# Kernel tuning notes

Hardware: AMD Instinct MI355X
Metric: run time of the kernel (lower is better)

The kernel has to match this reference:

```python
import jax, jax.numpy as jnp
import numpy as np

N_NODES = 50000
N_EDGES = 800000
IN_SIZE = 128
HIDDEN = 128   # out_size * 2
OUT_SIZE = 64


def setup_inputs() -> dict:
    key = jax.random.key(0)
    ks = jax.random.split(key, 6)
    h = jax.random.normal(ks[0], (N_NODES, IN_SIZE), dtype=jnp.float32)
    W1 = jax.random.normal(ks[1], (IN_SIZE, HIDDEN), dtype=jnp.float32) * (1.0 / np.sqrt(IN_SIZE))
    b1 = jnp.zeros((HIDDEN,), dtype=jnp.float32)
    W2 = jax.random.normal(ks[2], (HIDDEN, OUT_SIZE), dtype=jnp.float32) * (1.0 / np.sqrt(HIDDEN))
    b2 = jnp.zeros((OUT_SIZE,), dtype=jnp.float32)
    src = jax.random.randint(ks[3], (N_EDGES,), 0, N_NODES, dtype=jnp.int64)
    dst = jax.random.randint(ks[4], (N_EDGES,), 0, N_NODES, dtype=jnp.int64)
    return {"h": h, "W1": W1, "b1": b1, "W2": W2, "b2": b2, "src": src, "dst": dst}


def _norms(src, dst, n_nodes):
    # DGL GraphConv norm='both': scale by out_degree^{-1/2} (src side)
    # and in_degree^{-1/2} (dst side); zero degrees clamped to 1.
    ones = jnp.ones(src.shape, dtype=jnp.float32)
    out_deg = jnp.maximum(jax.ops.segment_sum(ones, src, num_segments=n_nodes), 1.0)
    in_deg = jnp.maximum(jax.ops.segment_sum(ones, dst, num_segments=n_nodes), 1.0)
    return (out_deg ** -0.5)[:, None], (in_deg ** -0.5)[:, None]


def _graph_conv(x, W, b, src, dst, norm_out, norm_in, n_nodes):
    # h' = D_in^{-1/2} A D_out^{-1/2} x W + b
    x = x * norm_out                                   # [N, F]
    agg = jax.ops.segment_sum(x[src], dst, num_segments=n_nodes)  # SpMM: [N, F]
    return (agg * norm_in) @ W + b


def reference(h, W1, b1, W2, b2, src, dst):
    n_nodes = h.shape[0]
    norm_out, norm_in = _norms(src, dst, n_nodes)
    h = jax.nn.relu(_graph_conv(h, W1, b1, src, dst, norm_out, norm_in, n_nodes))
    h = jax.nn.relu(_graph_conv(h, W2, b2, src, dst, norm_out, norm_in, n_nodes))
    return h
```

## Files before the change

kernel.cpp:

```cpp
#include <hip/hip_runtime.h>

#define N_NODES 50000
#define N_EDGES 800000
#define IN_SIZE 128
#define HIDDEN 128
#define OUT_SIZE 64

#define CHUNKS 128
#define CHUNK_EDGES 6250
#define GEMMA_TILES 1563
#define NBS 196

static __device__ inline unsigned pack_bf16x2(float a, float b) {
    unsigned ua = __float_as_uint(a);
    unsigned ub = __float_as_uint(b);
    unsigned ra = (ua + 0x7fffu + ((ua >> 16) & 1u)) >> 16;
    unsigned rb = (ub + 0x7fffu + ((ub >> 16) & 1u)) & 0xffff0000u;
    return ra | rb;
}

static __device__ inline unsigned pack_f16x2(float a, float b) {
    _Float16 ha = (_Float16)a, hb = (_Float16)b;
    unsigned short ua = __builtin_bit_cast(unsigned short, ha);
    unsigned short ub = __builtin_bit_cast(unsigned short, hb);
    return (unsigned)ua | ((unsigned)ub << 16);
}

static __device__ inline float2 unpack_f16x2(unsigned u) {
    _Float16 lo = __builtin_bit_cast(_Float16, (unsigned short)(u & 0xffffu));
    _Float16 hi = __builtin_bit_cast(_Float16, (unsigned short)(u >> 16));
    return make_float2((float)lo, (float)hi);
}

__global__ __launch_bounds__(1024) void hist_kernel(const int* __restrict__ src,
                                                    const int* __restrict__ dst,
                                                    unsigned char* __restrict__ cntD,
                                                    unsigned char* __restrict__ cntS,
                                                    unsigned char* __restrict__ rp) {
    __shared__ unsigned hD[12500];
    __shared__ unsigned hS[12500];
    const int t = threadIdx.x;
    const int c = blockIdx.x;

    for (int i = t; i < 12500; i += 1024) { hD[i] = 0u; hS[i] = 0u; }
    __syncthreads();

    const int base = c * CHUNK_EDGES;
    for (int i = t; i < CHUNK_EDGES; i += 1024) {
        int e = base + i;
        int d = dst[e];
        int s = src[e];
        unsigned shd = (unsigned)(d & 3) * 8u;
        unsigned old = atomicAdd(&hD[d >> 2], 1u << shd);
        rp[e] = (unsigned char)((old >> shd) & 0xffu);
        atomicAdd(&hS[s >> 2], 1u << ((unsigned)(s & 3) * 8u));
    }
    __syncthreads();

    unsigned* gD = (unsigned*)cntD + (size_t)c * 12500;
    unsigned* gS = (unsigned*)cntS + (size_t)c * 12500;
    for (int i = t; i < 12500; i += 1024) { gD[i] = hD[i]; gS[i] = hS[i]; }
}

__global__ __launch_bounds__(256) void deg_scan_kernel(unsigned char* __restrict__ cntD,
                                                       const unsigned char* __restrict__ cntS,
                                                       int* __restrict__ row_ptr,
                                                       int* __restrict__ bsum,
                                                       float* __restrict__ norm_out,
                                                       float* __restrict__ norm_in) {
    const int t = threadIdx.x, lane = t & 63, w = t >> 6;
    const int n = blockIdx.x * 256 + t;
    unsigned sumD = 0u, sumS = 0u;
    if (n < N_NODES) {
        #pragma unroll 4
        for (int c = 0; c < CHUNKS; ++c) {
            size_t idx = (size_t)c * 50000 + n;
            unsigned v = cntD[idx];
            cntD[idx] = (unsigned char)sumD;
            sumD += v;
            sumS += cntS[idx];
        }
        norm_in[n]  = rsqrtf((float)(sumD ? sumD : 1u));
        norm_out[n] = rsqrtf((float)(sumS ? sumS : 1u));
    }
    __shared__ int wsum[4];
    int v = (n < N_NODES) ? (int)sumD : 0;
    int incl = v;
    #pragma unroll
    for (int d = 1; d < 64; d <<= 1) {
        int u = __shfl_up(incl, d, 64);
        if (lane >= d) incl += u;
    }
    if (lane == 63) wsum[w] = incl;
    __syncthreads();
    int woff = 0, total = 0;
    #pragma unroll
    for (int j = 0; j < 4; ++j) {
        int s = wsum[j];
        if (j < w) woff += s;
        total += s;
    }
    if (n < N_NODES) row_ptr[n] = woff + incl - v;
    if (t == 0) bsum[blockIdx.x] = total;
}

__global__ __launch_bounds__(64) void scan2_kernel(int* __restrict__ bsum,
                                                   int* __restrict__ row_ptr) {
    const int lane = threadIdx.x;
    int carry = 0;
    for (int base = 0; base < NBS; base += 64) {
        int t = base + lane;
        int v = (t < NBS) ? bsum[t] : 0;
        int incl = v;
        #pragma unroll
        for (int d = 1; d < 64; d <<= 1) {
            int u = __shfl_up(incl, d, 64);
            if (lane >= d) incl += u;
        }
        int excl = carry + incl - v;
        if (t < NBS) bsum[t] = excl;
        if (t == NBS - 1) row_ptr[N_NODES] = N_EDGES - excl;
        carry += __shfl(incl, 63, 64);
    }
}

__global__ __launch_bounds__(256) void gemmA_kernel(const float* __restrict__ h,
                                                    const float* __restrict__ W1,
                                                    unsigned short* __restrict__ t1) {
    __shared__ float sA[32][128];
    __shared__ float sW[32][128];

    const int tile = blockIdx.x;
    const int t  = threadIdx.x;
    const int tx = t & 31;
    const int ty = t >> 5;
    const int n0 = tile * 32;

    for (int i = t; i < 1024; i += 256) {
        int n = i >> 5, c = i & 31;
        int gn = n0 + n;
        float4 v = make_float4(0.f, 0.f, 0.f, 0.f);
        if (gn < N_NODES) v = ((const float4*)(h + (size_t)gn * 128))[c];
        ((float4*)sA[n])[c] = v;
    }

    float4 acc[4];
    #pragma unroll
    for (int i = 0; i < 4; ++i) acc[i] = make_float4(0.f, 0.f, 0.f, 0.f);

    for (int kc = 0; kc < 4; ++kc) {
        __syncthreads();
        for (int i = t; i < 1024; i += 256) {
            int k = i >> 5, c = i & 31;
            ((float4*)sW[k])[c] = ((const float4*)(W1 + (size_t)(kc * 32 + k) * 128))[c];
        }
        __syncthreads();
        #pragma unroll 8
        for (int k = 0; k < 32; ++k) {
            float4 w = ((float4*)sW[k])[tx];
            #pragma unroll
            for (int ni = 0; ni < 4; ++ni) {
                float a = sA[ty * 4 + ni][kc * 32 + k];
                acc[ni].x = fmaf(a, w.x, acc[ni].x);
                acc[ni].y = fmaf(a, w.y, acc[ni].y);
                acc[ni].z = fmaf(a, w.z, acc[ni].z);
                acc[ni].w = fmaf(a, w.w, acc[ni].w);
            }
        }
    }

    #pragma unroll
    for (int ni = 0; ni < 4; ++ni) {
        int gn = n0 + ty * 4 + ni;
        if (gn < N_NODES) {
            uint2 p;
            p.x = pack_bf16x2(acc[ni].x, acc[ni].y);
            p.y = pack_bf16x2(acc[ni].z, acc[ni].w);
            ((uint2*)(t1 + (size_t)gn * 128))[tx] = p;
        }
    }
}

__global__ __launch_bounds__(256) void place_kernel(const int* __restrict__ src,
                                                    const int* __restrict__ dst,
                                                    const int* __restrict__ row_ptr,
                                                    const int* __restrict__ bsum,
                                                    const unsigned char* __restrict__ cntD,
                                                    const unsigned char* __restrict__ rp,
                                                    int* __restrict__ eidx) {
    int e = blockIdx.x * 256 + threadIdx.x;
    if (e < N_EDGES) {
        int d = dst[e];
        int c = e / CHUNK_EDGES;
        int pos = row_ptr[d] + bsum[d >> 8] + (int)cntD[(size_t)c * 50000 + d] + (int)rp[e];
        eidx[pos] = src[e];
    }
}

__global__ __launch_bounds__(256) void gemmB_kernel(const float* __restrict__ h1p,
                                                    const float* __restrict__ W2,
                                                    unsigned short* __restrict__ t2h) {
    __shared__ float sA[32][128];
    __shared__ float sW[128][64];
    const int t  = threadIdx.x;
    const int tx = t & 15;
    const int ty = t >> 4;
    const int n0 = blockIdx.x * 32;

    for (int i = t; i < 1024; i += 256) {
        int n = i >> 5, c = i & 31;
        int gn = n0 + n;
        float4 v = make_float4(0.f, 0.f, 0.f, 0.f);
        if (gn < N_NODES) v = ((const float4*)(h1p + (size_t)gn * 128))[c];
        ((float4*)sA[n])[c] = v;
    }
    for (int i = t; i < 2048; i += 256) {
        int k = i >> 4, c = i & 15;
        ((float4*)sW[k])[c] = ((const float4*)(W2 + (size_t)k * 64))[c];
    }
    __syncthreads();

    float4 a0 = make_float4(0.f, 0.f, 0.f, 0.f);
    float4 a1 = make_float4(0.f, 0.f, 0.f, 0.f);
    #pragma unroll 8
    for (int k = 0; k < 128; ++k) {
        float4 w = ((float4*)sW[k])[tx];
        float x0 = sA[ty * 2 + 0][k];
        float x1 = sA[ty * 2 + 1][k];
        a0.x = fmaf(x0, w.x, a0.x); a0.y = fmaf(x0, w.y, a0.y);
        a0.z = fmaf(x0, w.z, a0.z); a0.w = fmaf(x0, w.w, a0.w);
        a1.x = fmaf(x1, w.x, a1.x); a1.y = fmaf(x1, w.y, a1.y);
        a1.z = fmaf(x1, w.z, a1.z); a1.w = fmaf(x1, w.w, a1.w);
    }

    #pragma unroll
    for (int ni = 0; ni < 2; ++ni) {
        int gn = n0 + ty * 2 + ni;
        if (gn < N_NODES) {
            float4 a = ni ? a1 : a0;
            uint2 p;
            p.x = pack_f16x2(a.x, a.y);
            p.y = pack_f16x2(a.z, a.w);
            ((uint2*)(t2h + (size_t)gn * 64))[tx] = p;
        }
    }
}

__global__ __launch_bounds__(256) void pull128_kernel(const unsigned short* __restrict__ xb,
                                                      const int* __restrict__ row_ptr,
                                                      const int* __restrict__ bsum,
                                                      const int* __restrict__ eidx,
                                                      const float* __restrict__ b1,
                                                      const float* __restrict__ norm_in,
                                                      const float* __restrict__ norm_out,
                                                      float* __restrict__ out) {
    int node = blockIdx.x * 4 + (threadIdx.x >> 6);
    node = __builtin_amdgcn_readfirstlane(node);
    const int lane = threadIdx.x & 63;
    const int beg = __builtin_amdgcn_readfirstlane(row_ptr[node] + bsum[node >> 8]);
    const int end = __builtin_amdgcn_readfirstlane(row_ptr[node + 1] + bsum[(node + 1) >> 8]);

    float2 acc0 = make_float2(0.f, 0.f);
    float2 acc1 = make_float2(0.f, 0.f);
    float2 acc2 = make_float2(0.f, 0.f);
    float2 acc3 = make_float2(0.f, 0.f);

    for (int base = beg; base < end; base += 64) {
        const int cnt = min(64, end - base);
        int my_e = 0;
        float my_n = 0.f;
        if (lane < cnt) {
            my_e = eidx[base + lane];
            my_n = norm_out[my_e];
        }
        int k = 0;
        for (; k + 7 < cnt; k += 8) {
            int s0 = __builtin_amdgcn_readlane(my_e, k);
            int s1 = __builtin_amdgcn_readlane(my_e, k + 1);
            int s2 = __builtin_amdgcn_readlane(my_e, k + 2);
            int s3 = __builtin_amdgcn_readlane(my_e, k + 3);
            int s4 = __builtin_amdgcn_readlane(my_e, k + 4);
            int s5 = __builtin_amdgcn_readlane(my_e, k + 5);
            int s6 = __builtin_amdgcn_readlane(my_e, k + 6);
            int s7 = __builtin_amdgcn_readlane(my_e, k + 7);
            float n0 = __int_as_float(__builtin_amdgcn_readlane(__float_as_int(my_n), k));
            float n1 = __int_as_float(__builtin_amdgcn_readlane(__float_as_int(my_n), k + 1));
            float n2 = __int_as_float(__builtin_amdgcn_readlane(__float_as_int(my_n), k + 2));
            float n3 = __int_as_float(__builtin_amdgcn_readlane(__float_as_int(my_n), k + 3));
            float n4 = __int_as_float(__builtin_amdgcn_readlane(__float_as_int(my_n), k + 4));
            float n5 = __int_as_float(__builtin_amdgcn_readlane(__float_as_int(my_n), k + 5));
            float n6 = __int_as_float(__builtin_amdgcn_readlane(__float_as_int(my_n), k + 6));
            float n7 = __int_as_float(__builtin_amdgcn_readlane(__float_as_int(my_n), k + 7));
            unsigned u0 = ((const unsigned*)(xb + (size_t)s0 * 128))[lane];
            unsigned u1 = ((const unsigned*)(xb + (size_t)s1 * 128))[lane];
            unsigned u2 = ((const unsigned*)(xb + (size_t)s2 * 128))[lane];
            unsigned u3 = ((const unsigned*)(xb + (size_t)s3 * 128))[lane];
            unsigned u4 = ((const unsigned*)(xb + (size_t)s4 * 128))[lane];
            unsigned u5 = ((const unsigned*)(xb + (size_t)s5 * 128))[lane];
            unsigned u6 = ((const unsigned*)(xb + (size_t)s6 * 128))[lane];
            unsigned u7 = ((const unsigned*)(xb + (size_t)s7 * 128))[lane];
            acc0.x = fmaf(__uint_as_float(u0 << 16), n0, acc0.x);
            acc0.y = fmaf(__uint_as_float(u0 & 0xffff0000u), n0, acc0.y);
            acc1.x = fmaf(__uint_as_float(u1 << 16), n1, acc1.x);
            acc1.y = fmaf(__uint_as_float(u1 & 0xffff0000u), n1, acc1.y);
            acc2.x = fmaf(__uint_as_float(u2 << 16), n2, acc2.x);
            acc2.y = fmaf(__uint_as_float(u2 & 0xffff0000u), n2, acc2.y);
            acc3.x = fmaf(__uint_as_float(u3 << 16), n3, acc3.x);
            acc3.y = fmaf(__uint_as_float(u3 & 0xffff0000u), n3, acc3.y);
            acc0.x = fmaf(__uint_as_float(u4 << 16), n4, acc0.x);
            acc0.y = fmaf(__uint_as_float(u4 & 0xffff0000u), n4, acc0.y);
            acc1.x = fmaf(__uint_as_float(u5 << 16), n5, acc1.x);
            acc1.y = fmaf(__uint_as_float(u5 & 0xffff0000u), n5, acc1.y);
            acc2.x = fmaf(__uint_as_float(u6 << 16), n6, acc2.x);
            acc2.y = fmaf(__uint_as_float(u6 & 0xffff0000u), n6, acc2.y);
            acc3.x = fmaf(__uint_as_float(u7 << 16), n7, acc3.x);
            acc3.y = fmaf(__uint_as_float(u7 & 0xffff0000u), n7, acc3.y);
        }
        for (; k + 3 < cnt; k += 4) {
            int s0 = __builtin_amdgcn_readlane(my_e, k);
            int s1 = __builtin_amdgcn_readlane(my_e, k + 1);
            int s2 = __builtin_amdgcn_readlane(my_e, k + 2);
            int s3 = __builtin_amdgcn_readlane(my_e, k + 3);
            float n0 = __int_as_float(__builtin_amdgcn_readlane(__float_as_int(my_n), k));
            float n1 = __int_as_float(__builtin_amdgcn_readlane(__float_as_int(my_n), k + 1));
            float n2 = __int_as_float(__builtin_amdgcn_readlane(__float_as_int(my_n), k + 2));
            float n3 = __int_as_float(__builtin_amdgcn_readlane(__float_as_int(my_n), k + 3));
            unsigned u0 = ((const unsigned*)(xb + (size_t)s0 * 128))[lane];
            unsigned u1 = ((const unsigned*)(xb + (size_t)s1 * 128))[lane];
            unsigned u2 = ((const unsigned*)(xb + (size_t)s2 * 128))[lane];
            unsigned u3 = ((const unsigned*)(xb + (size_t)s3 * 128))[lane];
            acc0.x = fmaf(__uint_as_float(u0 << 16), n0, acc0.x);
            acc0.y = fmaf(__uint_as_float(u0 & 0xffff0000u), n0, acc0.y);
            acc1.x = fmaf(__uint_as_float(u1 << 16), n1, acc1.x);
            acc1.y = fmaf(__uint_as_float(u1 & 0xffff0000u), n1, acc1.y);
            acc2.x = fmaf(__uint_as_float(u2 << 16), n2, acc2.x);
            acc2.y = fmaf(__uint_as_float(u2 & 0xffff0000u), n2, acc2.y);
            acc3.x = fmaf(__uint_as_float(u3 << 16), n3, acc3.x);
            acc3.y = fmaf(__uint_as_float(u3 & 0xffff0000u), n3, acc3.y);
        }
        for (; k < cnt; ++k) {
            int s0 = __builtin_amdgcn_readlane(my_e, k);
            float n0 = __int_as_float(__builtin_amdgcn_readlane(__float_as_int(my_n), k));
            unsigned u0 = ((const unsigned*)(xb + (size_t)s0 * 128))[lane];
            acc0.x = fmaf(__uint_as_float(u0 << 16), n0, acc0.x);
            acc0.y = fmaf(__uint_as_float(u0 & 0xffff0000u), n0, acc0.y);
        }
    }

    float ni = norm_in[node];
    float no = norm_out[node];
    float2 bb = ((const float2*)b1)[lane];
    float sx = (acc0.x + acc1.x) + (acc2.x + acc3.x);
    float sy = (acc0.y + acc1.y) + (acc2.y + acc3.y);
    float2 r;
    r.x = fmaxf(fmaf(sx, ni, bb.x), 0.f) * no;
    r.y = fmaxf(fmaf(sy, ni, bb.y), 0.f) * no;
    ((float2*)(out + (size_t)node * 128))[lane] = r;
}

__global__ __launch_bounds__(256) void pull64_kernel(const unsigned* __restrict__ x,
                                                     const int* __restrict__ row_ptr,
                                                     const int* __restrict__ bsum,
                                                     const int* __restrict__ eidx,
                                                     const float* __restrict__ b2,
                                                     const float* __restrict__ norm_in,
                                                     float* __restrict__ out) {
    int node = blockIdx.x * 4 + (threadIdx.x >> 6);
    node = __builtin_amdgcn_readfirstlane(node);
    const int lane = threadIdx.x & 63;
    const int half = lane >> 5;
    const int fl = lane & 31;
    const int beg = __builtin_amdgcn_readfirstlane(row_ptr[node] + bsum[node >> 8]);
    const int end = __builtin_amdgcn_readfirstlane(row_ptr[node + 1] + bsum[(node + 1) >> 8]);

    float2 a0 = make_float2(0.f, 0.f);
    float2 a1 = make_float2(0.f, 0.f);
    float2 a2 = make_float2(0.f, 0.f);
    float2 a3 = make_float2(0.f, 0.f);

    for (int base = beg; base < end; base += 64) {
        const int cnt = min(64, end - base);
        int my_e = (lane < cnt) ? eidx[base + lane] : 0;
        int k = 0;
        for (; k + 7 < cnt; k += 8) {
            int sa0 = __builtin_amdgcn_readlane(my_e, k);
            int sb0 = __builtin_amdgcn_readlane(my_e, k + 1);
            int sa1 = __builtin_amdgcn_readlane(my_e, k + 2);
            int sb1 = __builtin_amdgcn_readlane(my_e, k + 3);
            int sa2 = __builtin_amdgcn_readlane(my_e, k + 4);
            int sb2 = __builtin_amdgcn_readlane(my_e, k + 5);
            int sa3 = __builtin_amdgcn_readlane(my_e, k + 6);
            int sb3 = __builtin_amdgcn_readlane(my_e, k + 7);
            int e0 = half ? sb0 : sa0;
            int e1 = half ? sb1 : sa1;
            int e2 = half ? sb2 : sa2;
            int e3 = half ? sb3 : sa3;
            unsigned u0 = x[(size_t)e0 * 32 + fl];
            unsigned u1 = x[(size_t)e1 * 32 + fl];
            unsigned u2 = x[(size_t)e2 * 32 + fl];
            unsigned u3 = x[(size_t)e3 * 32 + fl];
            float2 v0 = unpack_f16x2(u0);
            float2 v1 = unpack_f16x2(u1);
            float2 v2 = unpack_f16x2(u2);
            float2 v3 = unpack_f16x2(u3);
            a0.x += v0.x; a0.y += v0.y;
            a1.x += v1.x; a1.y += v1.y;
            a2.x += v2.x; a2.y += v2.y;
            a3.x += v3.x; a3.y += v3.y;
        }
        for (; k + 1 < cnt; k += 2) {
            int sa = __builtin_amdgcn_readlane(my_e, k);
            int sb = __builtin_amdgcn_readlane(my_e, k + 1);
            int e0 = half ? sb : sa;
            unsigned u = x[(size_t)e0 * 32 + fl];
            float2 v = unpack_f16x2(u);
            a0.x += v.x; a0.y += v.y;
        }
        if (k < cnt) {
            int sa = __builtin_amdgcn_readlane(my_e, k);
            if (half == 0) {
                unsigned u = x[(size_t)sa * 32 + fl];
                float2 v = unpack_f16x2(u);
                a0.x += v.x; a0.y += v.y;
            }
        }
    }

    float ax = (a0.x + a1.x) + (a2.x + a3.x);
    float ay = (a0.y + a1.y) + (a2.y + a3.y);
    ax += __shfl_xor(ax, 32, 64);
    ay += __shfl_xor(ay, 32, 64);
    if (half == 0) {
        float ni = norm_in[node];
        float2 bb = ((const float2*)b2)[fl];
        float2 r;
        r.x = fmaxf(fmaf(ax, ni, bb.x), 0.f);
        r.y = fmaxf(fmaf(ay, ni, bb.y), 0.f);
        ((float2*)(out + (size_t)node * 64))[fl] = r;
    }
}

extern "C" void kernel_launch(void* const* d_in, const int* in_sizes, int n_in,
                              void* d_out, int out_size, void* d_ws, size_t ws_size,
                              hipStream_t stream) {
    const float* h  = (const float*)d_in[0];
    const float* W1 = (const float*)d_in[1];
    const float* b1 = (const float*)d_in[2];
    const float* W2 = (const float*)d_in[3];
    const float* b2 = (const float*)d_in[4];
    const int* src  = (const int*)d_in[5];
    const int* dst  = (const int*)d_in[6];
    float* out = (float*)d_out;

    char* ws = (char*)d_ws;
    size_t off = 0;
    auto alloc = [&](size_t bytes) {
        void* p = ws + off;
        off = (off + bytes + 255) & ~(size_t)255;
        return p;
    };
    float* norm_out   = (float*)alloc(N_NODES * sizeof(float));
    float* norm_in    = (float*)alloc(N_NODES * sizeof(float));
    int* row_ptr      = (int*)alloc((N_NODES + 1) * sizeof(int));
    int* bsum         = (int*)alloc(NBS * sizeof(int));
    int* eidx         = (int*)alloc((size_t)N_EDGES * sizeof(int));
    unsigned short* t1 = (unsigned short*)alloc((size_t)N_NODES * 128 * sizeof(short));
    float* h1p        = (float*)alloc((size_t)N_NODES * 128 * sizeof(float));

    unsigned char* cntD = (unsigned char*)h1p;
    unsigned char* cntS = cntD + (size_t)CHUNKS * 50000;
    unsigned char* rp   = cntS + (size_t)CHUNKS * 50000;
    unsigned short* t2h = t1;

    hist_kernel<<<CHUNKS, 1024, 0, stream>>>(src, dst, cntD, cntS, rp);

    gemmA_kernel<<<GEMMA_TILES, 256, 0, stream>>>(h, W1, t1);

    deg_scan_kernel<<<NBS, 256, 0, stream>>>(cntD, cntS, row_ptr, bsum, norm_out, norm_in);

    scan2_kernel<<<1, 64, 0, stream>>>(bsum, row_ptr);

    place_kernel<<<(N_EDGES + 255) / 256, 256, 0, stream>>>(src, dst, row_ptr, bsum, cntD, rp, eidx);

    pull128_kernel<<<N_NODES / 4, 256, 0, stream>>>(t1, row_ptr, bsum, eidx, b1,
                                                    norm_in, norm_out, h1p);

    gemmB_kernel<<<(N_NODES + 31) / 32, 256, 0, stream>>>(h1p, W2, t2h);
    pull64_kernel<<<N_NODES / 4, 256, 0, stream>>>((const unsigned*)t2h, row_ptr, bsum, eidx,
                                                   b2, norm_in, out);
}
```

Baseline: 227.1 us.

## Fuse histogram and first GEMM into one launch; half-wave edge split in pull128

Merges the edge histogram kernel and the first dense transform into a single launch: low block indices build per-chunk histograms, the rest compute four 32-row GEMM tiles each using partitioned 128KB shared memory. This lets the histogram work overlap with the GEMM and removes a launch. The 128-wide gather kernel now has each half-wave process a different edge with 8-byte loads, then combines the halves via a cross-lane shuffle. This gives fewer load instructions per edge, at the cost of a reduction and larger per-block shared memory.

```diff
diff --git a/kernel.cpp b/kernel.cpp
--- a/kernel.cpp
+++ b/kernel.cpp
@@ -9,6 +9,8 @@
 #define CHUNKS 128
 #define CHUNK_EDGES 6250
 #define GEMMA_TILES 1563
+#define GEMMA_SUPER 391
+#define FUSED_GRID (CHUNKS + GEMMA_SUPER)
 #define NBS 196
 
 static __device__ inline unsigned pack_bf16x2(float a, float b) {
@@ -32,34 +34,98 @@
     return make_float2((float)lo, (float)hi);
 }
 
-__global__ __launch_bounds__(1024) void hist_kernel(const int* __restrict__ src,
-                                                    const int* __restrict__ dst,
-                                                    unsigned char* __restrict__ cntD,
-                                                    unsigned char* __restrict__ cntS,
-                                                    unsigned char* __restrict__ rp) {
-    __shared__ unsigned hD[12500];
-    __shared__ unsigned hS[12500];
-    const int t = threadIdx.x;
-    const int c = blockIdx.x;
-
-    for (int i = t; i < 12500; i += 1024) { hD[i] = 0u; hS[i] = 0u; }
-    __syncthreads();
-
-    const int base = c * CHUNK_EDGES;
-    for (int i = t; i < CHUNK_EDGES; i += 1024) {
-        int e = base + i;
-        int d = dst[e];
-        int s = src[e];
-        unsigned shd = (unsigned)(d & 3) * 8u;
-        unsigned old = atomicAdd(&hD[d >> 2], 1u << shd);
-        rp[e] = (unsigned char)((old >> shd) & 0xffu);
-        atomicAdd(&hS[s >> 2], 1u << ((unsigned)(s & 3) * 8u));
-    }
-    __syncthreads();
-
-    unsigned* gD = (unsigned*)cntD + (size_t)c * 12500;
-    unsigned* gS = (unsigned*)cntS + (size_t)c * 12500;
-    for (int i = t; i < 12500; i += 1024) { gD[i] = hD[i]; gS[i] = hS[i]; }
+static __device__ inline float bf_lo(unsigned w) { return __uint_as_float(w << 16); }
+static __device__ inline float bf_hi(unsigned w) { return __uint_as_float(w & 0xffff0000u); }
+
+__global__ __launch_bounds__(1024) void fused_hist_gemmA(const int* __restrict__ src,
+                                                         const int* __restrict__ dst,
+                                                         unsigned char* __restrict__ cntD,
+                                                         unsigned char* __restrict__ cntS,
+                                                         unsigned char* __restrict__ rp,
+                                                         const float* __restrict__ h,
+                                                         const float* __restrict__ W1,
+                                                         unsigned short* __restrict__ t1) {
+    __shared__ __align__(16) unsigned char smem[131072];
+    const int b = blockIdx.x;
+
+    if (b < CHUNKS) {
+        unsigned* hD = (unsigned*)smem;
+        unsigned* hS = hD + 12500;
+        const int t = threadIdx.x;
+        for (int i = t; i < 12500; i += 1024) { hD[i] = 0u; hS[i] = 0u; }
+        __syncthreads();
+        const int base = b * CHUNK_EDGES;
+        for (int i = t; i < CHUNK_EDGES; i += 1024) {
+            int e = base + i;
+            int d = dst[e];
+            int s = src[e];
+            unsigned shd = (unsigned)(d & 3) * 8u;
+            unsigned old = atomicAdd(&hD[d >> 2], 1u << shd);
+            rp[e] = (unsigned char)((old >> shd) & 0xffu);
+            atomicAdd(&hS[s >> 2], 1u << ((unsigned)(s & 3) * 8u));
+        }
+        __syncthreads();
+        unsigned* gD = (unsigned*)cntD + (size_t)b * 12500;
+        unsigned* gS = (unsigned*)cntS + (size_t)b * 12500;
+        for (int i = t; i < 12500; i += 1024) { gD[i] = hD[i]; gS[i] = hS[i]; }
+        return;
+    }
+
+    const int sub = threadIdx.x >> 8;
+    const int t   = threadIdx.x & 255;
+    int tile = (b - CHUNKS) * 4 + sub;
+    if (tile >= GEMMA_TILES) tile = GEMMA_TILES - 1;
+
+    float* sA = (float*)(smem + (size_t)sub * 32768);
+    float* sW = sA + 32 * 128;
+
+    const int tx = t & 31;
+    const int ty = t >> 5;
+    const int n0 = tile * 32;
+
+    for (int i = t; i < 1024; i += 256) {
+        int n = i >> 5, c = i & 31;
+        int gn = n0 + n;
+        float4 v = make_float4(0.f, 0.f, 0.f, 0.f);
+        if (gn < N_NODES) v = ((const float4*)(h + (size_t)gn * 128))[c];
+        ((float4*)(sA + n * 128))[c] = v;
+    }
+
+    float4 acc[4];
+    #pragma unroll
+    for (int i = 0; i < 4; ++i) acc[i] = make_float4(0.f, 0.f, 0.f, 0.f);
+
+    for (int kc = 0; kc < 4; ++kc) {
+        __syncthreads();
+        for (int i = t; i < 1024; i += 256) {
+            int k = i >> 5, c = i & 31;
+            ((float4*)(sW + k * 128))[c] = ((const float4*)(W1 + (size_t)(kc * 32 + k) * 128))[c];
+        }
+        __syncthreads();
+        #pragma unroll 8
+        for (int k = 0; k < 32; ++k) {
+            float4 w = ((float4*)(sW + k * 128))[tx];
+            #pragma unroll
+            for (int ni = 0; ni < 4; ++ni) {
+                float a = sA[(ty * 4 + ni) * 128 + kc * 32 + k];
+                acc[ni].x = fmaf(a, w.x, acc[ni].x);
+                acc[ni].y = fmaf(a, w.y, acc[ni].y);
+                acc[ni].z = fmaf(a, w.z, acc[ni].z);
+                acc[ni].w = fmaf(a, w.w, acc[ni].w);
+            }
+        }
+    }
+
+    #pragma unroll
+    for (int ni = 0; ni < 4; ++ni) {
+        int gn = n0 + ty * 4 + ni;
+        if (gn < N_NODES) {
+            uint2 p;
+            p.x = pack_bf16x2(acc[ni].x, acc[ni].y);
+            p.y = pack_bf16x2(acc[ni].z, acc[ni].w);
+            ((uint2*)(t1 + (size_t)gn * 128))[tx] = p;
+        }
+    }
 }
 
 __global__ __launch_bounds__(256) void deg_scan_kernel(unsigned char* __restrict__ cntD,
@@ -124,63 +190,6 @@
     }
 }
 
-__global__ __launch_bounds__(256) void gemmA_kernel(const float* __restrict__ h,
-                                                    const float* __restrict__ W1,
-                                                    unsigned short* __restrict__ t1) {
-    __shared__ float sA[32][128];
-    __shared__ float sW[32][128];
-
-    const int tile = blockIdx.x;
-    const int t  = threadIdx.x;
-    const int tx = t & 31;
-    const int ty = t >> 5;
-    const int n0 = tile * 32;
-
-    for (int i = t; i < 1024; i += 256) {
-        int n = i >> 5, c = i & 31;
-        int gn = n0 + n;
-        float4 v = make_float4(0.f, 0.f, 0.f, 0.f);
-        if (gn < N_NODES) v = ((const float4*)(h + (size_t)gn * 128))[c];
-        ((float4*)sA[n])[c] = v;
-    }
-
-    float4 acc[4];
-    #pragma unroll
-    for (int i = 0; i < 4; ++i) acc[i] = make_float4(0.f, 0.f, 0.f, 0.f);
-
-    for (int kc = 0; kc < 4; ++kc) {
-        __syncthreads();
-        for (int i = t; i < 1024; i += 256) {
-            int k = i >> 5, c = i & 31;
-            ((float4*)sW[k])[c] = ((const float4*)(W1 + (size_t)(kc * 32 + k) * 128))[c];
-        }
-        __syncthreads();
-        #pragma unroll 8
-        for (int k = 0; k < 32; ++k) {
-            float4 w = ((float4*)sW[k])[tx];
-            #pragma unroll
-            for (int ni = 0; ni < 4; ++ni) {
-                float a = sA[ty * 4 + ni][kc * 32 + k];
-                acc[ni].x = fmaf(a, w.x, acc[ni].x);
-                acc[ni].y = fmaf(a, w.y, acc[ni].y);
-                acc[ni].z = fmaf(a, w.z, acc[ni].z);
-                acc[ni].w = fmaf(a, w.w, acc[ni].w);
-            }
-        }
-    }
-
-    #pragma unroll
-    for (int ni = 0; ni < 4; ++ni) {
-        int gn = n0 + ty * 4 + ni;
-        if (gn < N_NODES) {
-            uint2 p;
-            p.x = pack_bf16x2(acc[ni].x, acc[ni].y);
-            p.y = pack_bf16x2(acc[ni].z, acc[ni].w);
-            ((uint2*)(t1 + (size_t)gn * 128))[tx] = p;
-        }
-    }
-}
-
 __global__ __launch_bounds__(256) void place_kernel(const int* __restrict__ src,
                                                     const int* __restrict__ dst,
                                                     const int* __restrict__ row_ptr,
@@ -257,13 +266,15 @@
     int node = blockIdx.x * 4 + (threadIdx.x >> 6);
     node = __builtin_amdgcn_readfirstlane(node);
     const int lane = threadIdx.x & 63;
+    const int half = lane >> 5;
+    const int fl = lane & 31;
     const int beg = __builtin_amdgcn_readfirstlane(row_ptr[node] + bsum[node >> 8]);
     const int end = __builtin_amdgcn_readfirstlane(row_ptr[node + 1] + bsum[(node + 1) >> 8]);
 
-    float2 acc0 = make_float2(0.f, 0.f);
-    float2 acc1 = make_float2(0.f, 0.f);
-    float2 acc2 = make_float2(0.f, 0.f);
-    float2 acc3 = make_float2(0.f, 0.f);
+    float4 acc0 = make_float4(0.f, 0.f, 0.f, 0.f);
+    float4 acc1 = make_float4(0.f, 0.f, 0.f, 0.f);
+    float4 acc2 = make_float4(0.f, 0.f, 0.f, 0.f);
+    float4 acc3 = make_float4(0.f, 0.f, 0.f, 0.f);
 
     for (int base = beg; base < end; base += 64) {
         const int cnt = min(64, end - base);
@@ -275,87 +286,92 @@
         }
         int k = 0;
         for (; k + 7 < cnt; k += 8) {
-            int s0 = __builtin_amdgcn_readlane(my_e, k);
-            int s1 = __builtin_amdgcn_readlane(my_e, k + 1);
-            int s2 = __builtin_amdgcn_readlane(my_e, k + 2);
-            int s3 = __builtin_amdgcn_readlane(my_e, k + 3);
-            int s4 = __builtin_amdgcn_readlane(my_e, k + 4);
-            int s5 = __builtin_amdgcn_readlane(my_e, k + 5);
-            int s6 = __builtin_amdgcn_readlane(my_e, k + 6);
-            int s7 = __builtin_amdgcn_readlane(my_e, k + 7);
-            float n0 = __int_as_float(__builtin_amdgcn_readlane(__float_as_int(my_n), k));
-            float n1 = __int_as_float(__builtin_amdgcn_readlane(__float_as_int(my_n), k + 1));
-            float n2 = __int_as_float(__builtin_amdgcn_readlane(__float_as_int(my_n), k + 2));
-            float n3 = __int_as_float(__builtin_amdgcn_readlane(__float_as_int(my_n), k + 3));
-            float n4 = __int_as_float(__builtin_amdgcn_readlane(__float_as_int(my_n), k + 4));
-            float n5 = __int_as_float(__builtin_amdgcn_readlane(__float_as_int(my_n), k + 5));
-            float n6 = __int_as_float(__builtin_amdgcn_readlane(__float_as_int(my_n), k + 6));
-            float n7 = __int_as_float(__builtin_amdgcn_readlane(__float_as_int(my_n), k + 7));
-            unsigned u0 = ((const unsigned*)(xb + (size_t)s0 * 128))[lane];
-            unsigned u1 = ((const unsigned*)(xb + (size_t)s1 * 128))[lane];
-            unsigned u2 = ((const unsigned*)(xb + (size_t)s2 * 128))[lane];
-            unsigned u3 = ((const unsigned*)(xb + (size_t)s3 * 128))[lane];
-            unsigned u4 = ((const unsigned*)(xb + (size_t)s4 * 128))[lane];
-            unsigned u5 = ((const unsigned*)(xb + (size_t)s5 * 128))[lane];
-            unsigned u6 = ((const unsigned*)(xb + (size_t)s6 * 128))[lane];
-            unsigned u7 = ((const unsigned*)(xb + (size_t)s7 * 128))[lane];
-            acc0.x = fmaf(__uint_as_float(u0 << 16), n0, acc0.x);
-            acc0.y = fmaf(__uint_as_float(u0 & 0xffff0000u), n0, acc0.y);
-            acc1.x = fmaf(__uint_as_float(u1 << 16), n1, acc1.x);
-            acc1.y = fmaf(__uint_as_float(u1 & 0xffff0000u), n1, acc1.y);
-            acc2.x = fmaf(__uint_as_float(u2 << 16), n2, acc2.x);
-            acc2.y = fmaf(__uint_as_float(u2 & 0xffff0000u), n2, acc2.y);
-            acc3.x = fmaf(__uint_as_float(u3 << 16), n3, acc3.x);
-            acc3.y = fmaf(__uint_as_float(u3 & 0xffff0000u), n3, acc3.y);
-            acc0.x = fmaf(__uint_as_float(u4 << 16), n4, acc0.x);
-            acc0.y = fmaf(__uint_as_float(u4 & 0xffff0000u), n4, acc0.y);
-            acc1.x = fmaf(__uint_as_float(u5 << 16), n5, acc1.x);
-            acc1.y = fmaf(__uint_as_float(u5 & 0xffff0000u), n5, acc1.y);
-            acc2.x = fmaf(__uint_as_float(u6 << 16), n6, acc2.x);
-            acc2.y = fmaf(__uint_as_float(u6 & 0xffff0000u), n6, acc2.y);
-            acc3.x = fmaf(__uint_as_float(u7 << 16), n7, acc3.x);
-            acc3.y = fmaf(__uint_as_float(u7 & 0xffff0000u), n7, acc3.y);
-        }
-        for (; k + 3 < cnt; k += 4) {
-            int s0 = __builtin_amdgcn_readlane(my_e, k);
-            int s1 = __builtin_amdgcn_readlane(my_e, k + 1);
-            int s2 = __builtin_amdgcn_readlane(my_e, k + 2);
-            int s3 = __builtin_amdgcn_readlane(my_e, k + 3);
-            float n0 = __int_as_float(__builtin_amdgcn_readlane(__float_as_int(my_n), k));
-            float n1 = __int_as_float(__builtin_amdgcn_readlane(__float_as_int(my_n), k + 1));
-            float n2 = __int_as_float(__builtin_amdgcn_readlane(__float_as_int(my_n), k + 2));
-            float n3 = __int_as_float(__builtin_amdgcn_readlane(__float_as_int(my_n), k + 3));
-            unsigned u0 = ((const unsigned*)(xb + (size_t)s0 * 128))[lane];
-            unsigned u1 = ((const unsigned*)(xb + (size_t)s1 * 128))[lane];
-            unsigned u2 = ((const unsigned*)(xb + (size_t)s2 * 128))[lane];
-            unsigned u3 = ((const unsigned*)(xb + (size_t)s3 * 128))[lane];
-            acc0.x = fmaf(__uint_as_float(u0 << 16), n0, acc0.x);
-            acc0.y = fmaf(__uint_as_float(u0 & 0xffff0000u), n0, acc0.y);
-            acc1.x = fmaf(__uint_as_float(u1 << 16), n1, acc1.x);
-            acc1.y = fmaf(__uint_as_float(u1 & 0xffff0000u), n1, acc1.y);
-            acc2.x = fmaf(__uint_as_float(u2 << 16), n2, acc2.x);
-            acc2.y = fmaf(__uint_as_float(u2 & 0xffff0000u), n2, acc2.y);
-            acc3.x = fmaf(__uint_as_float(u3 << 16), n3, acc3.x);
-            acc3.y = fmaf(__uint_as_float(u3 & 0xffff0000u), n3, acc3.y);
-        }
-        for (; k < cnt; ++k) {
-            int s0 = __builtin_amdgcn_readlane(my_e, k);
-            float n0 = __int_as_float(__builtin_amdgcn_readlane(__float_as_int(my_n), k));
-            unsigned u0 = ((const unsigned*)(xb + (size_t)s0 * 128))[lane];
-            acc0.x = fmaf(__uint_as_float(u0 << 16), n0, acc0.x);
-            acc0.y = fmaf(__uint_as_float(u0 & 0xffff0000u), n0, acc0.y);
-        }
-    }
-
-    float ni = norm_in[node];
-    float no = norm_out[node];
-    float2 bb = ((const float2*)b1)[lane];
-    float sx = (acc0.x + acc1.x) + (acc2.x + acc3.x);
-    float sy = (acc0.y + acc1.y) + (acc2.y + acc3.y);
-    float2 r;
-    r.x = fmaxf(fmaf(sx, ni, bb.x), 0.f) * no;
-    r.y = fmaxf(fmaf(sy, ni, bb.y), 0.f) * no;
-    ((float2*)(out + (size_t)node * 128))[lane] = r;
+            int sl0 = __builtin_amdgcn_readlane(my_e, k);
+            int sh0 = __builtin_amdgcn_readlane(my_e, k + 1);
+            int sl1 = __builtin_amdgcn_readlane(my_e, k + 2);
+            int sh1 = __builtin_amdgcn_readlane(my_e, k + 3);
+            int sl2 = __builtin_amdgcn_readlane(my_e, k + 4);
+            int sh2 = __builtin_amdgcn_readlane(my_e, k + 5);
+            int sl3 = __builtin_amdgcn_readlane(my_e, k + 6);
+            int sh3 = __builtin_amdgcn_readlane(my_e, k + 7);
+            float nl0 = __int_as_float(__builtin_amdgcn_readlane(__float_as_int(my_n), k));
+            float nh0 = __int_as_float(__builtin_amdgcn_readlane(__float_as_int(my_n), k + 1));
+            float nl1 = __int_as_float(__builtin_amdgcn_readlane(__float_as_int(my_n), k + 2));
+            float nh1 = __int_as_float(__builtin_amdgcn_readlane(__float_as_int(my_n), k + 3));
+            float nl2 = __int_as_float(__builtin_amdgcn_readlane(__float_as_int(my_n), k + 4));
+            float nh2 = __int_as_float(__builtin_amdgcn_readlane(__float_as_int(my_n), k + 5));
+            float nl3 = __int_as_float(__builtin_amdgcn_readlane(__float_as_int(my_n), k + 6));
+            float nh3 = __int_as_float(__builtin_amdgcn_readlane(__float_as_int(my_n), k + 7));
+            int s0 = half ? sh0 : sl0;  float n0 = half ? nh0 : nl0;
+            int s1 = half ? sh1 : sl1;  float n1 = half ? nh1 : nl1;
+            int s2 = half ? sh2 : sl2;  float n2 = half ? nh2 : nl2;
+            int s3 = half ? sh3 : sl3;  float n3 = half ? nh3 : nl3;
+            uint2 u0 = ((const uint2*)(xb + (size_t)s0 * 128))[fl];
+            uint2 u1 = ((const uint2*)(xb + (size_t)s1 * 128))[fl];
+            uint2 u2 = ((const uint2*)(xb + (size_t)s2 * 128))[fl];
+            uint2 u3 = ((const uint2*)(xb + (size_t)s3 * 128))[fl];
+            acc0.x = fmaf(bf_lo(u0.x), n0, acc0.x);
+            acc0.y = fmaf(bf_hi(u0.x), n0, acc0.y);
+            acc0.z = fmaf(bf_lo(u0.y), n0, acc0.z);
+            acc0.w = fmaf(bf_hi(u0.y), n0, acc0.w);
+            acc1.x = fmaf(bf_lo(u1.x), n1, acc1.x);
+            acc1.y = fmaf(bf_hi(u1.x), n1, acc1.y);
+            acc1.z = fmaf(bf_lo(u1.y), n1, acc1.z);
+            acc1.w = fmaf(bf_hi(u1.y), n1, acc1.w);
+            acc2.x = fmaf(bf_lo(u2.x), n2, acc2.x);
+            acc2.y = fmaf(bf_hi(u2.x), n2, acc2.y);
+            acc2.z = fmaf(bf_lo(u2.y), n2, acc2.z);
+            acc2.w = fmaf(bf_hi(u2.y), n2, acc2.w);
+            acc3.x = fmaf(bf_lo(u3.x), n3, acc3.x);
+            acc3.y = fmaf(bf_hi(u3.x), n3, acc3.y);
+            acc3.z = fmaf(bf_lo(u3.y), n3, acc3.z);
+            acc3.w = fmaf(bf_hi(u3.y), n3, acc3.w);
+        }
+        for (; k + 1 < cnt; k += 2) {
+            int sl = __builtin_amdgcn_readlane(my_e, k);
+            int sh = __builtin_amdgcn_readlane(my_e, k + 1);
+            float nl = __int_as_float(__builtin_amdgcn_readlane(__float_as_int(my_n), k));
+            float nh = __int_as_float(__builtin_amdgcn_readlane(__float_as_int(my_n), k + 1));
+            int s = half ? sh : sl;  float n = half ? nh : nl;
+            uint2 u = ((const uint2*)(xb + (size_t)s * 128))[fl];
+            acc0.x = fmaf(bf_lo(u.x), n, acc0.x);
+            acc0.y = fmaf(bf_hi(u.x), n, acc0.y);
+            acc0.z = fmaf(bf_lo(u.y), n, acc0.z);
+            acc0.w = fmaf(bf_hi(u.y), n, acc0.w);
+        }
+        if (k < cnt) {
+            int sl = __builtin_amdgcn_readlane(my_e, k);
+            float nl = __int_as_float(__builtin_amdgcn_readlane(__float_as_int(my_n), k));
+            float n = half ? 0.f : nl;
+            uint2 u = ((const uint2*)(xb + (size_t)sl * 128))[fl];
+            acc0.x = fmaf(bf_lo(u.x), n, acc0.x);
+            acc0.y = fmaf(bf_hi(u.x), n, acc0.y);
+            acc0.z = fmaf(bf_lo(u.y), n, acc0.z);
+            acc0.w = fmaf(bf_hi(u.y), n, acc0.w);
+        }
+    }
+
+    float4 s;
+    s.x = (acc0.x + acc1.x) + (acc2.x + acc3.x);
+    s.y = (acc0.y + acc1.y) + (acc2.y + acc3.y);
+    s.z = (acc0.z + acc1.z) + (acc2.z + acc3.z);
+    s.w = (acc0.w + acc1.w) + (acc2.w + acc3.w);
+    s.x += __shfl_xor(s.x, 32, 64);
+    s.y += __shfl_xor(s.y, 32, 64);
+    s.z += __shfl_xor(s.z, 32, 64);
+    s.w += __shfl_xor(s.w, 32, 64);
+
+    if (half == 0) {
+        float ni = norm_in[node];
+        float no = norm_out[node];
+        float4 bb = ((const float4*)b1)[fl];
+        float4 r;
+        r.x = fmaxf(fmaf(s.x, ni, bb.x), 0.f) * no;
+        r.y = fmaxf(fmaf(s.y, ni, bb.y), 0.f) * no;
+        r.z = fmaxf(fmaf(s.z, ni, bb.z), 0.f) * no;
+        r.w = fmaxf(fmaf(s.w, ni, bb.w), 0.f) * no;
+        ((float4*)(out + (size_t)node * 128))[fl] = r;
+    }
 }
 
 __global__ __launch_bounds__(256) void pull64_kernel(const unsigned* __restrict__ x,
@@ -472,9 +488,7 @@
     unsigned char* rp   = cntS + (size_t)CHUNKS * 50000;
     unsigned short* t2h = t1;
 
-    hist_kernel<<<CHUNKS, 1024, 0, stream>>>(src, dst, cntD, cntS, rp);
-
-    gemmA_kernel<<<GEMMA_TILES, 256, 0, stream>>>(h, W1, t1);
+    fused_hist_gemmA<<<FUSED_GRID, 1024, 0, stream>>>(src, dst, cntD, cntS, rp, h, W1, t1);
 
     deg_scan_kernel<<<NBS, 256, 0, stream>>>(cntD, cntS, row_ptr, bsum, norm_out, norm_in);
 
```

Measured after the change: 228.9 us. Within noise of the previous version (+0.8%).

## Restructure gemmA to stream h rows from registers and vectorize gemmB LDS reads

Applied to the files above, without the earlier changes.

gemmA now loads all of W1 into shared memory once per block. Each wavefront handles 8 rows, streaming h directly from global memory into registers with a one-step prefetch, so the per-k-chunk syncs and the shared staging of h are gone. gemmB reads its A operand from shared memory as float4 across four k steps instead of scalar loads per k, which cuts LDS instruction count. The 64KB shared W tile may reduce occupancy in gemmA, and per-lane global float4 reads of h rows are strided rather than coalesced.

```diff
diff --git a/kernel.cpp b/kernel.cpp
--- a/kernel.cpp
+++ b/kernel.cpp
@@ -60,6 +60,68 @@
     unsigned* gD = (unsigned*)cntD + (size_t)c * 12500;
     unsigned* gS = (unsigned*)cntS + (size_t)c * 12500;
     for (int i = t; i < 12500; i += 1024) { gD[i] = hD[i]; gS[i] = hS[i]; }
+}
+
+__global__ __launch_bounds__(256) void gemmA_kernel(const float* __restrict__ h,
+                                                    const float* __restrict__ W1,
+                                                    unsigned short* __restrict__ t1) {
+    __shared__ __align__(16) float sW[128][128];
+    const int t = threadIdx.x;
+
+    for (int i = t; i < 4096; i += 256)
+        ((float4*)sW)[i] = ((const float4*)W1)[i];
+
+    const int wv   = __builtin_amdgcn_readfirstlane(t >> 6);
+    const int lane = t & 63;
+    const int n0   = blockIdx.x * 32 + wv * 8;
+    const int c0   = lane * 2;
+
+    const float* hr[8];
+    #pragma unroll
+    for (int r = 0; r < 8; ++r) {
+        int gn = n0 + r;
+        if (gn > N_NODES - 1) gn = N_NODES - 1;
+        hr[r] = h + (size_t)gn * 128;
+    }
+
+    float4 a_cur[8], a_nxt[8];
+    #pragma unroll
+    for (int r = 0; r < 8; ++r) a_cur[r] = *(const float4*)(hr[r]);
+
+    __syncthreads();
+
+    float2 acc[8];
+    #pragma unroll
+    for (int r = 0; r < 8; ++r) acc[r] = make_float2(0.f, 0.f);
+
+    for (int k4 = 0; k4 < 128; k4 += 4) {
+        if (k4 + 4 < 128) {
+            #pragma unroll
+            for (int r = 0; r < 8; ++r) a_nxt[r] = *(const float4*)(hr[r] + k4 + 4);
+        }
+        #pragma unroll
+        for (int kk = 0; kk < 4; ++kk) {
+            float2 w = *(const float2*)&sW[k4 + kk][c0];
+            #pragma unroll
+            for (int r = 0; r < 8; ++r) {
+                float a = (kk == 0) ? a_cur[r].x : (kk == 1) ? a_cur[r].y
+                        : (kk == 2) ? a_cur[r].z : a_cur[r].w;
+                acc[r].x = fmaf(a, w.x, acc[r].x);
+                acc[r].y = fmaf(a, w.y, acc[r].y);
+            }
+        }
+        #pragma unroll
+        for (int r = 0; r < 8; ++r) a_cur[r] = a_nxt[r];
+    }
+
+    #pragma unroll
+    for (int r = 0; r < 8; ++r) {
+        int gn = n0 + r;
+        if (gn < N_NODES) {
+            unsigned p = pack_bf16x2(acc[r].x, acc[r].y);
+            ((unsigned*)(t1 + (size_t)gn * 128))[lane] = p;
+        }
+    }
 }
 
 __global__ __launch_bounds__(256) void deg_scan_kernel(unsigned char* __restrict__ cntD,
@@ -124,63 +186,6 @@
     }
 }
 
-__global__ __launch_bounds__(256) void gemmA_kernel(const float* __restrict__ h,
-                                                    const float* __restrict__ W1,
-                                                    unsigned short* __restrict__ t1) {
-    __shared__ float sA[32][128];
-    __shared__ float sW[32][128];
-
-    const int tile = blockIdx.x;
-    const int t  = threadIdx.x;
-    const int tx = t & 31;
-    const int ty = t >> 5;
-    const int n0 = tile * 32;
-
-    for (int i = t; i < 1024; i += 256) {
-        int n = i >> 5, c = i & 31;
-        int gn = n0 + n;
-        float4 v = make_float4(0.f, 0.f, 0.f, 0.f);
-        if (gn < N_NODES) v = ((const float4*)(h + (size_t)gn * 128))[c];
-        ((float4*)sA[n])[c] = v;
-    }
-
-    float4 acc[4];
-    #pragma unroll
-    for (int i = 0; i < 4; ++i) acc[i] = make_float4(0.f, 0.f, 0.f, 0.f);
-
-    for (int kc = 0; kc < 4; ++kc) {
-        __syncthreads();
-        for (int i = t; i < 1024; i += 256) {
-            int k = i >> 5, c = i & 31;
-            ((float4*)sW[k])[c] = ((const float4*)(W1 + (size_t)(kc * 32 + k) * 128))[c];
-        }
-        __syncthreads();
-        #pragma unroll 8
-        for (int k = 0; k < 32; ++k) {
-            float4 w = ((float4*)sW[k])[tx];
-            #pragma unroll
-            for (int ni = 0; ni < 4; ++ni) {
-                float a = sA[ty * 4 + ni][kc * 32 + k];
-                acc[ni].x = fmaf(a, w.x, acc[ni].x);
-                acc[ni].y = fmaf(a, w.y, acc[ni].y);
-                acc[ni].z = fmaf(a, w.z, acc[ni].z);
-                acc[ni].w = fmaf(a, w.w, acc[ni].w);
-            }
-        }
-    }
-
-    #pragma unroll
-    for (int ni = 0; ni < 4; ++ni) {
-        int gn = n0 + ty * 4 + ni;
-        if (gn < N_NODES) {
-            uint2 p;
-            p.x = pack_bf16x2(acc[ni].x, acc[ni].y);
-            p.y = pack_bf16x2(acc[ni].z, acc[ni].w);
-            ((uint2*)(t1 + (size_t)gn * 128))[tx] = p;
-        }
-    }
-}
-
 __global__ __launch_bounds__(256) void place_kernel(const int* __restrict__ src,
                                                     const int* __restrict__ dst,
                                                     const int* __restrict__ row_ptr,
@@ -222,15 +227,19 @@
 
     float4 a0 = make_float4(0.f, 0.f, 0.f, 0.f);
     float4 a1 = make_float4(0.f, 0.f, 0.f, 0.f);
-    #pragma unroll 8
-    for (int k = 0; k < 128; ++k) {
-        float4 w = ((float4*)sW[k])[tx];
-        float x0 = sA[ty * 2 + 0][k];
-        float x1 = sA[ty * 2 + 1][k];
-        a0.x = fmaf(x0, w.x, a0.x); a0.y = fmaf(x0, w.y, a0.y);
-        a0.z = fmaf(x0, w.z, a0.z); a0.w = fmaf(x0, w.w, a0.w);
-        a1.x = fmaf(x1, w.x, a1.x); a1.y = fmaf(x1, w.y, a1.y);
-        a1.z = fmaf(x1, w.z, a1.z); a1.w = fmaf(x1, w.w, a1.w);
+    #pragma unroll 4
+    for (int k4 = 0; k4 < 128; k4 += 4) {
+        float x0[4], x1[4];
+        *(float4*)x0 = *(const float4*)&sA[ty * 2 + 0][k4];
+        *(float4*)x1 = *(const float4*)&sA[ty * 2 + 1][k4];
+        #pragma unroll
+        for (int kk = 0; kk < 4; ++kk) {
+            float4 w = ((float4*)sW[k4 + kk])[tx];
+            a0.x = fmaf(x0[kk], w.x, a0.x); a0.y = fmaf(x0[kk], w.y, a0.y);
+            a0.z = fmaf(x0[kk], w.z, a0.z); a0.w = fmaf(x0[kk], w.w, a0.w);
+            a1.x = fmaf(x1[kk], w.x, a1.x); a1.y = fmaf(x1[kk], w.y, a1.y);
+            a1.z = fmaf(x1[kk], w.z, a1.z); a1.w = fmaf(x1[kk], w.w, a1.w);
+        }
     }
 
     #pragma unroll
```

Result: slower. 253.1 us (+11.5%).
